# Optimization experiments

Measured on AMD Instinct MI355X. Metric: run time of the kernel, lower is better.

## Reference

```python
import jax, jax.numpy as jnp
import numpy as np

N_HEAD = 16  # from init_kwargs

def setup_inputs() -> dict:
    key = jax.random.key(0)
    k1, k2, k3 = jax.random.split(key, 3)
    B, T, C = 2, 2048, 1024
    x = jax.random.normal(k1, (B, T, C), dtype=jnp.float32)
    W_qkv = jax.random.normal(k2, (3 * C, C), dtype=jnp.float32) * (1.0 / np.sqrt(C))
    W_proj = jax.random.normal(k3, (C, C), dtype=jnp.float32) * (1.0 / np.sqrt(C))
    b_proj = jnp.zeros((C,), dtype=jnp.float32)
    return {"x": x, "W_qkv": W_qkv, "W_proj": W_proj, "b_proj": b_proj}

def reference(x, W_qkv, W_proj, b_proj):
    B, T, C = x.shape
    H = N_HEAD
    hs = C // H
    # QKV projection (bias=False), split heads
    qkv = (x @ W_qkv.T).reshape(B, T, 3, H, hs)
    q = jnp.transpose(qkv[:, :, 0], (0, 2, 1, 3))  # [B,H,T,hs]
    k = jnp.transpose(qkv[:, :, 1], (0, 2, 1, 3))
    v = jnp.transpose(qkv[:, :, 2], (0, 2, 1, 3))
    scale = np.float32(1.0 / np.sqrt(hs))
    s = jnp.einsum('bhqd,bhkd->bhqk', q, k) * scale  # [B,H,T,T]
    # sp2norm: softplus weights, causal-masked, normalized by row L2 norm
    w = jax.nn.softplus(s)
    causal = jnp.tril(jnp.ones((T, T), dtype=bool))
    w = jnp.where(causal[None, None], w, jnp.float32(0.0))
    norm = jnp.sqrt(jnp.sum(w * w, axis=-1, keepdims=True))  # [B,H,T,1]
    out = jnp.einsum('bhqk,bhkd->bhqd', w, v) / norm  # [B,H,T,hs]
    out = jnp.transpose(out, (0, 2, 1, 3)).reshape(B, T, C)
    return out @ W_proj.T + b_proj
```

## Files before the change

kernel.cpp:

```cpp
#include <hip/hip_runtime.h>
#include <cstdint>
#include <cstddef>

typedef __bf16 bf16_t;
typedef __bf16 bf16x8 __attribute__((ext_vector_type(8)));
typedef __bf16 bf16x4 __attribute__((ext_vector_type(4)));
typedef float  f32x4  __attribute__((ext_vector_type(4)));

#define MFMA_BF16(a, b, c) __builtin_amdgcn_mfma_f32_16x16x32_bf16((a), (b), (c), 0, 0, 0)

__device__ __forceinline__ void async_load16(const void* g, void* l) {
    __builtin_amdgcn_global_load_lds((const __attribute__((address_space(1))) void*)g,
                                     (__attribute__((address_space(3))) void*)l,
                                     16, 0, 0);
}

#define SWZ(r, cg) ((((r) << 3) | ((cg) ^ ((r) & 7))) << 3)

#define Bq   2
#define Tq   2048
#define Cq   1024
#define Hq   16
#define HSq  64
#define Mrows 4096

__global__ __launch_bounds__(256)
void cvt_all(const float* __restrict__ x, const float* __restrict__ wqkv,
             const float* __restrict__ wproj,
             bf16_t* __restrict__ xb, bf16_t* __restrict__ wqkvb,
             bf16_t* __restrict__ wprojb) {
    size_t gid = (size_t)blockIdx.x * 256 + threadIdx.x;
    const float* src; bf16_t* dst; size_t off;
    if (gid < 1048576)      { src = x;     dst = xb;     off = gid; }
    else if (gid < 1835008) { src = wqkv;  dst = wqkvb;  off = gid - 1048576; }
    else                    { src = wproj; dst = wprojb; off = gid - 1835008; }
    float4 v = ((const float4*)src)[off];
    bf16x4 o;
    o[0] = (bf16_t)v.x; o[1] = (bf16_t)v.y; o[2] = (bf16_t)v.z; o[3] = (bf16_t)v.w;
    *(bf16x4*)(dst + off * 4) = o;
}

template <int BM, int EPI>
__global__ __launch_bounds__(256)
void gemm_bt(const bf16_t* __restrict__ A, const bf16_t* __restrict__ B,
             void* __restrict__ Cout, const float* __restrict__ bias,
             bf16_t* __restrict__ qc, bf16_t* __restrict__ kc, bf16_t* __restrict__ vtp,
             int M, int N, int K) {
    constexpr int MR = BM / 32;
    __shared__ __align__(16) bf16_t As[BM * 32];
    __shared__ __align__(16) bf16_t Bs[128 * 32];

    const int tid  = threadIdx.x;
    const int wave = tid >> 6;
    const int lane = tid & 63;
    const int m0 = blockIdx.y * BM;
    const int n0 = blockIdx.x * 128;
    const int wm = (wave >> 1) * (BM / 2);
    const int wn = (wave & 1) * 64;
    const int lrow = lane & 15;
    const int lko  = (lane >> 4) * 8;

    f32x4 acc[MR][4] = {};

    const bf16_t* Ag = A + (size_t)m0 * K;
    const bf16_t* Bg = B + (size_t)n0 * K;
    const int c0 = tid, c1 = tid + 256;

    for (int k0 = 0; k0 < K; k0 += 32) {
        async_load16(Ag + (size_t)(c0 >> 2) * K + k0 + (c0 & 3) * 8, &As[c0 * 8]);
        if (BM == 128)
            async_load16(Ag + (size_t)(c1 >> 2) * K + k0 + (c1 & 3) * 8, &As[c1 * 8]);
        async_load16(Bg + (size_t)(c0 >> 2) * K + k0 + (c0 & 3) * 8, &Bs[c0 * 8]);
        async_load16(Bg + (size_t)(c1 >> 2) * K + k0 + (c1 & 3) * 8, &Bs[c1 * 8]);
        __syncthreads();

        bf16x8 af[MR], bfr[4];
        #pragma unroll
        for (int r = 0; r < MR; r++) af[r] = *(const bf16x8*)&As[(wm + r * 16 + lrow) * 32 + lko];
        #pragma unroll
        for (int c = 0; c < 4; c++) bfr[c] = *(const bf16x8*)&Bs[(wn + c * 16 + lrow) * 32 + lko];
        #pragma unroll
        for (int r = 0; r < MR; r++)
            #pragma unroll
            for (int c = 0; c < 4; c++)
                acc[r][c] = MFMA_BF16(af[r], bfr[c], acc[r][c]);
        __syncthreads();
    }

    const int er = (lane >> 4) * 4;
    const int ec = lane & 15;
    #pragma unroll
    for (int r = 0; r < MR; r++) {
        #pragma unroll
        for (int c = 0; c < 4; c++) {
            int m = m0 + wm + r * 16 + er;
            int n = n0 + wn + c * 16 + ec;
            if (EPI == 1) {
                #pragma unroll
                for (int v = 0; v < 4; v++)
                    ((float*)Cout)[(size_t)(m + v) * N + n] = acc[r][c][v] + bias[n];
            } else {
                int bb = m >> 11, t = m & 2047;
                if (n < 1024) {
                    #pragma unroll
                    for (int v = 0; v < 4; v++)
                        qc[(size_t)(m + v) * 1024 + n] = (bf16_t)acc[r][c][v];
                } else if (n < 2048) {
                    int h = (n - 1024) >> 6, d = (n - 1024) & 63;
                    bf16_t* p = kc + ((size_t)(bb * 16 + h) * Tq + t) * 64 + d;
                    #pragma unroll
                    for (int v = 0; v < 4; v++) p[v * 64] = (bf16_t)acc[r][c][v];
                } else {
                    int h = (n - 2048) >> 6, d = (n - 2048) & 63;
                    bf16x4 o;
                    #pragma unroll
                    for (int v = 0; v < 4; v++) o[v] = (bf16_t)acc[r][c][v];
                    *(bf16x4*)&vtp[((size_t)(bb * 16 + h) * 64 + d) * Tq + t] = o;
                }
            }
        }
    }
}

__global__ __launch_bounds__(256)
void attn_kernel(const bf16_t* __restrict__ Qc, const bf16_t* __restrict__ Kc,
                 const bf16_t* __restrict__ Vt,
                 bf16_t* __restrict__ Op0, bf16_t* __restrict__ Op1,
                 bf16_t* __restrict__ Op2, bf16_t* __restrict__ Op3,
                 float* __restrict__ n2part) {
    __shared__ __align__(16) bf16_t Ks[64 * 64];
    __shared__ __align__(16) bf16_t Vs[64 * 64];
    __shared__ __align__(16) bf16_t Ws[64 * 64];

    const int tid = threadIdx.x;
    const int wave = tid >> 6;
    const int lane = tid & 63;
    const int lrow = lane & 15;
    const int lg   = lane >> 4;
    const int er = lg * 4;
    const int ec = lane & 15;

    const int raw     = blockIdx.x;
    const int qi      = 31 - (raw >> 2);
    const int quarter = raw & 3;
    const int q0      = qi * 64;
    const int bh = blockIdx.y;
    const int b = bh >> 4, h = bh & 15;

    const int nt = qi + 1;
    const int lo = (quarter * nt) >> 2;
    const int hi = ((quarter + 1) * nt) >> 2;

    const bf16_t* Qb = Qc + (size_t)b * Tq * Cq + h * 64;
    const bf16_t* Kb = Kc + (size_t)bh * Tq * 64;
    const bf16_t* Vb = Vt + (size_t)bh * 64 * Tq;

    bf16x8 qf[2];
    {
        const bf16_t* qrow = Qb + (size_t)(q0 + wave * 16 + lrow) * Cq + lg * 8;
        qf[0] = *(const bf16x8*)(qrow);
        qf[1] = *(const bf16x8*)(qrow + 32);
    }

    const int s0 = tid, s1 = tid + 256;
    const int r0 = s0 >> 3, cg0 = (s0 & 7) ^ (r0 & 7);
    const int r1 = s1 >> 3, cg1 = (s1 & 7) ^ (r1 & 7);

    bf16x8 kr0, kr1, vr0, vr1;
    if (lo < hi) {
        const int key0 = lo * 64;
        kr0 = *(const bf16x8*)&Kb[(size_t)(key0 + r0) * 64 + cg0 * 8];
        kr1 = *(const bf16x8*)&Kb[(size_t)(key0 + r1) * 64 + cg1 * 8];
        vr0 = *(const bf16x8*)&Vb[(size_t)r0 * Tq + key0 + cg0 * 8];
        vr1 = *(const bf16x8*)&Vb[(size_t)r1 * Tq + key0 + cg1 * 8];
    }

    f32x4 oacc[4] = {};
    float n2 = 0.f;
    const float C1 = 0.18033688f;

    for (int kt = lo; kt < hi; kt++) {
        __syncthreads();
        *(bf16x8*)&Ks[s0 * 8] = kr0;
        *(bf16x8*)&Ks[s1 * 8] = kr1;
        *(bf16x8*)&Vs[s0 * 8] = vr0;
        *(bf16x8*)&Vs[s1 * 8] = vr1;
        __syncthreads();

        if (kt + 1 < hi) {
            const int k1 = (kt + 1) * 64;
            kr0 = *(const bf16x8*)&Kb[(size_t)(k1 + r0) * 64 + cg0 * 8];
            kr1 = *(const bf16x8*)&Kb[(size_t)(k1 + r1) * 64 + cg1 * 8];
            vr0 = *(const bf16x8*)&Vb[(size_t)r0 * Tq + k1 + cg0 * 8];
            vr1 = *(const bf16x8*)&Vb[(size_t)r1 * Tq + k1 + cg1 * 8];
        }

        f32x4 sacc[4];
        #pragma unroll
        for (int j = 0; j < 4; j++) {
            int r = j * 16 + lrow;
            bf16x8 kf0 = *(const bf16x8*)&Ks[SWZ(r, lg)];
            bf16x8 kf1 = *(const bf16x8*)&Ks[SWZ(r, 4 + lg)];
            f32x4 z = {};
            z = MFMA_BF16(kf0, qf[0], z);
            sacc[j] = MFMA_BF16(kf1, qf[1], z);
        }

        const bool diag = (kt == qi);
        #pragma unroll
        for (int j = 0; j < 4; j++) {
            bf16x4 wb;
            #pragma unroll
            for (int v = 0; v < 4; v++) {
                float t = sacc[j][v] * C1;
                float e = __builtin_amdgcn_exp2f(-fabsf(t));
                float w = fmaxf(t, 0.f) + __builtin_amdgcn_logf(1.f + e);
                if (diag && (j * 16 + er + v > wave * 16 + ec)) w = 0.f;
                n2 += w * w;
                wb[v] = (bf16_t)w;
            }
            *(bf16x4*)&Ws[SWZ(wave * 16 + ec, 2 * j + (lg >> 1)) + (lg & 1) * 4] = wb;
        }

        #pragma unroll
        for (int s2 = 0; s2 < 2; s2++) {
            bf16x8 wf = *(const bf16x8*)&Ws[SWZ(wave * 16 + lrow, s2 * 4 + lg)];
            #pragma unroll
            for (int jd = 0; jd < 4; jd++) {
                bf16x8 vf = *(const bf16x8*)&Vs[SWZ(jd * 16 + lrow, s2 * 4 + lg)];
                oacc[jd] = MFMA_BF16(wf, vf, oacc[jd]);
            }
        }
    }

    n2 += __shfl_xor(n2, 16, 64);
    n2 += __shfl_xor(n2, 32, 64);

    bf16_t* Op = (quarter == 0 ? Op0 : quarter == 1 ? Op1 : quarter == 2 ? Op2 : Op3)
               + ((size_t)bh * 32 + qi) * 4096;
    #pragma unroll
    for (int jd = 0; jd < 4; jd++) {
        #pragma unroll
        for (int v = 0; v < 4; v++) {
            Op[(wave * 16 + er + v) * 64 + jd * 16 + ec] = (bf16_t)oacc[jd][v];
        }
    }
    if (lg == 0) {
        n2part[((size_t)quarter * 1024 + bh * 32 + qi) * 64 + wave * 16 + ec] = n2;
    }
}

__global__ __launch_bounds__(256)
void combine_kernel(const bf16_t* __restrict__ O0, const bf16_t* __restrict__ O1,
                    const bf16_t* __restrict__ O2, const bf16_t* __restrict__ O3,
                    const float* __restrict__ n2part, bf16_t* __restrict__ ao) {
    const int qi = blockIdx.x;
    const int bh = blockIdx.y;
    const int b = bh >> 4, h = bh & 15;
    const int t = threadIdx.x;
    const size_t base = ((size_t)bh * 32 + qi) * 4096;
    const float* np = n2part + ((size_t)bh * 32 + qi) * 64;
    #pragma unroll
    for (int i = 0; i < 2; i++) {
        int idx = i * 2048 + t * 8;
        int row = idx >> 6, col = idx & 63;
        bf16x8 a0 = *(const bf16x8*)(O0 + base + idx);
        bf16x8 a1 = *(const bf16x8*)(O1 + base + idx);
        bf16x8 a2 = *(const bf16x8*)(O2 + base + idx);
        bf16x8 a3 = *(const bf16x8*)(O3 + base + idx);
        float nsum = np[row] + np[(size_t)1024 * 64 + row]
                   + np[(size_t)2048 * 64 + row] + np[(size_t)3072 * 64 + row];
        float inv = rsqrtf(nsum);
        bf16x8 o;
        #pragma unroll
        for (int j = 0; j < 8; j++)
            o[j] = (bf16_t)(((float)a0[j] + (float)a1[j] + (float)a2[j] + (float)a3[j]) * inv);
        *(bf16x8*)(ao + (size_t)(b * Tq + qi * 64 + row) * Cq + h * HSq + col) = o;
    }
}

extern "C" void kernel_launch(void* const* d_in, const int* in_sizes, int n_in,
                              void* d_out, int out_size, void* d_ws, size_t ws_size,
                              hipStream_t stream) {
    const float* x     = (const float*)d_in[0];
    const float* wqkv  = (const float*)d_in[1];
    const float* wproj = (const float*)d_in[2];
    const float* bproj = (const float*)d_in[3];
    float* out = (float*)d_out;

    char* ws = (char*)d_ws;
    bf16_t* wprojb = (bf16_t*)(ws);
    bf16_t* xb     = (bf16_t*)(ws + ( 2u << 20));
    bf16_t* wqkvb  = (bf16_t*)(ws + (10u << 20));
    bf16_t* qcb    = (bf16_t*)(ws + (16u << 20));
    bf16_t* kcb    = (bf16_t*)(ws + (24u << 20));
    bf16_t* vtb    = (bf16_t*)(ws + (32u << 20));
    bf16_t* opart0 = (bf16_t*)(ws + ( 2u << 20));
    float*  n2part = (float*)(ws + (10u << 20));
    bf16_t* opart1 = (bf16_t*)(ws + (40u << 20));
    bf16_t* opart2 = (bf16_t*)(ws + (48u << 20));
    bf16_t* opart3 = (bf16_t*)(ws + (56u << 20));
    bf16_t* aob    = (bf16_t*)(ws + (24u << 20));

    cvt_all<<<8192, 256, 0, stream>>>(x, wqkv, wproj, xb, wqkvb, wprojb);

    gemm_bt<128, 2><<<dim3(24, 32), 256, 0, stream>>>(xb, wqkvb, nullptr, nullptr,
                                                      qcb, kcb, vtb, Mrows, 3 * Cq, Cq);
    attn_kernel<<<dim3(128, 32), 256, 0, stream>>>(qcb, kcb, vtb,
                                                   opart0, opart1, opart2, opart3, n2part);
    combine_kernel<<<dim3(32, 32), 256, 0, stream>>>(opart0, opart1, opart2, opart3,
                                                     n2part, aob);
    gemm_bt<64, 1><<<dim3(8, 64), 256, 0, stream>>>(aob, wprojb, (void*)out, bproj,
                                                    nullptr, nullptr, nullptr, Mrows, Cq, Cq);
}
```

Baseline: 196.1 us.

## Double GEMM K-tile to 64 and XOR-swizzle LDS layout

The bf16 GEMM now stages a K-depth of 64 per iteration instead of 32, which halves the number of barrier pairs and the loop overhead per unit of work. Each tile is stored in LDS with an XOR swizzle on 16-byte column groups, so the MFMA fragment reads avoid bank conflicts. LDS use per block doubles, which may lower occupancy. There is still no double buffering, so loads and compute remain serialized.

```diff
diff --git a/kernel.cpp b/kernel.cpp
--- a/kernel.cpp
+++ b/kernel.cpp
@@ -47,8 +47,9 @@
              bf16_t* __restrict__ qc, bf16_t* __restrict__ kc, bf16_t* __restrict__ vtp,
              int M, int N, int K) {
     constexpr int MR = BM / 32;
-    __shared__ __align__(16) bf16_t As[BM * 32];
-    __shared__ __align__(16) bf16_t Bs[128 * 32];
+    constexpr int ACH = BM * 8 / 256;
+    __shared__ __align__(16) bf16_t As[BM * 64];
+    __shared__ __align__(16) bf16_t Bs[128 * 64];
 
     const int tid  = threadIdx.x;
     const int wave = tid >> 6;
@@ -58,32 +59,43 @@
     const int wm = (wave >> 1) * (BM / 2);
     const int wn = (wave & 1) * 64;
     const int lrow = lane & 15;
-    const int lko  = (lane >> 4) * 8;
+    const int lg   = lane >> 4;
 
     f32x4 acc[MR][4] = {};
 
     const bf16_t* Ag = A + (size_t)m0 * K;
     const bf16_t* Bg = B + (size_t)n0 * K;
-    const int c0 = tid, c1 = tid + 256;
-
-    for (int k0 = 0; k0 < K; k0 += 32) {
-        async_load16(Ag + (size_t)(c0 >> 2) * K + k0 + (c0 & 3) * 8, &As[c0 * 8]);
-        if (BM == 128)
-            async_load16(Ag + (size_t)(c1 >> 2) * K + k0 + (c1 & 3) * 8, &As[c1 * 8]);
-        async_load16(Bg + (size_t)(c0 >> 2) * K + k0 + (c0 & 3) * 8, &Bs[c0 * 8]);
-        async_load16(Bg + (size_t)(c1 >> 2) * K + k0 + (c1 & 3) * 8, &Bs[c1 * 8]);
+
+    for (int k0 = 0; k0 < K; k0 += 64) {
+        #pragma unroll
+        for (int i = 0; i < ACH; i++) {
+            int s = i * 256 + tid;
+            int r = s >> 3, cg = (s & 7) ^ (r & 7);
+            async_load16(Ag + (size_t)r * K + k0 + cg * 8, &As[s * 8]);
+        }
+        #pragma unroll
+        for (int i = 0; i < 4; i++) {
+            int s = i * 256 + tid;
+            int r = s >> 3, cg = (s & 7) ^ (r & 7);
+            async_load16(Bg + (size_t)r * K + k0 + cg * 8, &Bs[s * 8]);
+        }
         __syncthreads();
 
-        bf16x8 af[MR], bfr[4];
-        #pragma unroll
-        for (int r = 0; r < MR; r++) af[r] = *(const bf16x8*)&As[(wm + r * 16 + lrow) * 32 + lko];
-        #pragma unroll
-        for (int c = 0; c < 4; c++) bfr[c] = *(const bf16x8*)&Bs[(wn + c * 16 + lrow) * 32 + lko];
-        #pragma unroll
-        for (int r = 0; r < MR; r++)
+        #pragma unroll
+        for (int kk = 0; kk < 2; kk++) {
+            bf16x8 af[MR], bfr[4];
+            #pragma unroll
+            for (int r = 0; r < MR; r++)
+                af[r] = *(const bf16x8*)&As[SWZ(wm + r * 16 + lrow, kk * 4 + lg)];
             #pragma unroll
             for (int c = 0; c < 4; c++)
-                acc[r][c] = MFMA_BF16(af[r], bfr[c], acc[r][c]);
+                bfr[c] = *(const bf16x8*)&Bs[SWZ(wn + c * 16 + lrow, kk * 4 + lg)];
+            #pragma unroll
+            for (int r = 0; r < MR; r++)
+                #pragma unroll
+                for (int c = 0; c < 4; c++)
+                    acc[r][c] = MFMA_BF16(af[r], bfr[c], acc[r][c]);
+        }
         __syncthreads();
     }
 
```

Result: faster. 188.0 us (-4.1%).
